# Performance work log

Measured on AMD Instinct MI355X. Metric: run time of the kernel, lower is better.

## Reference

```python
import jax, jax.numpy as jnp
import numpy as np

B, N, T, IN_DIM, OUT_DIM = 16, 500, 12, 2, 2
H, D, K, NH, NBLOCKS, T_OUT, GDEP = 64, 64, 10, 24, 2, 12, 2
H2 = 2 * H


def setup_inputs():
    key = jax.random.key(0)
    ks = iter(jax.random.split(key, 64))

    def rn(shape, s=1.0):
        return jax.random.normal(next(ks), shape, dtype=jnp.float32) * s

    def z(*shape):
        return jnp.zeros(shape, jnp.float32)

    sI = 1.0 / np.sqrt(IN_DIM)
    sH = 1.0 / np.sqrt(H)
    sH2 = 1.0 / np.sqrt(H2)
    sD = 1.0 / np.sqrt(D)
    adj = jax.random.uniform(next(ks), (N, N), dtype=jnp.float32)
    inp = {
        'x': rn((B, N, T, IN_DIM)),
        'weather': rn((B, T, 4)),
        'geo_adj': adj / adj.sum(1, keepdims=True),
        'fcx_W': rn((IN_DIM, H), sI), 'fcx_b': z(H),
        'env_cb': rn((K, D)), 'nodes_cb': rn((N, D)),
        'w_v': rn((D, K), sD), 'w_k': rn((D, D), sD), 'w_q': rn((D, D), sD),
        'core_W': rn((H, H * H), sH), 'core_b': z(H * H),
        'tcnN_Win': rn((K, H2, H2), sH2), 'tcnN_bin': z(K, H2),
        'tcnN_Wf': rn((K, NBLOCKS, 2, H2, H2), sH2), 'tcnN_bf': z(K, NBLOCKS, H2),
        'tcnN_Wg': rn((K, NBLOCKS, 2, H2, H2), sH2), 'tcnN_bg': z(K, NBLOCKS, H2),
        'tcnN_Wout': rn((K, H2, H), sH2), 'tcnN_bout': z(K, H),
        'tcnP_Win': rn((K, H2, H2), sH2), 'tcnP_bin': z(K, H2),
        'tcnP_Wf': rn((K, NBLOCKS, 2, H2, H2), sH2), 'tcnP_bf': z(K, NBLOCKS, H2),
        'tcnP_Wg': rn((K, NBLOCKS, 2, H2, H2), sH2), 'tcnP_bg': z(K, NBLOCKS, H2),
        'tcnP_Wout': rn((K, H2, H), sH2), 'tcnP_bout': z(K, H),
        'bn1_g': jnp.ones((H,), jnp.float32), 'bn1_b': z(H),
        'bnP_g': jnp.ones((H,), jnp.float32), 'bnP_b': z(H),
        'gcn1_W': rn((H, H), sH), 'gcn1_b': z(H),
        'gcn2_W': rn((H, H), sH), 'gcn2_b': z(H),
        'gcnp_W': rn((H, H), sH), 'gcnp_b': z(H),
        'nv_p1': rn((2 * NH, H)), 'nv_p2': rn((N, H)), 'nv_p3': rn((N, H)),
        'nv_pk': rn((H, H, H), sH),
        'out_W1': rn((T_OUT, H, 100), sH), 'out_b1': z(T_OUT, 100),
        'out_W2': rn((T_OUT, 100, OUT_DIM), 0.1), 'out_b2': z(T_OUT, OUT_DIM),
        't_pos': jax.random.randint(next(ks), (B, T, 2), 0, 7),
        'ind': jax.random.randint(next(ks), (B, T, 2), 0, 7),
    }
    return inp


def _tstep_emb(t, dim):
    half = dim // 2
    freqs = jnp.exp(-jnp.log(10000.0) * jnp.arange(half, dtype=jnp.float32) / half)
    a = t.astype(jnp.float32)[:, None] * freqs[None]
    return jnp.concatenate([jnp.cos(a), jnp.sin(a)], -1)


def _conv2(h, W, b, d):
    # causal kernel-2 dilated conv over time: h [B,N,T,C], W [2,C,Co] -> [B,N,T-d,Co]
    return (jnp.einsum('bntc,co->bnto', h[:, :, :-d], W[0])
            + jnp.einsum('bntc,co->bnto', h[:, :, d:], W[1]) + b)


def _tcn(xin, Win, bin_, Wf, bf, Wg, bg, Wout, bout):
    # gated dilated TCN (Graph-WaveNet style), per node over time
    h = jnp.einsum('bntc,co->bnto', xin, Win) + bin_
    for l in range(Wf.shape[0]):
        d = 2 ** l
        f = jnp.tanh(_conv2(h, Wf[l], bf[l], d))
        g = jax.nn.sigmoid(_conv2(h, Wg[l], bg[l], d))
        h = f * g + h[:, :, d:, :]
    return jnp.einsum('bntc,ch->bnth', h, Wout) + bout


def _bn(h, g, b):
    # BatchNorm1d over channels, stats over (batch, nodes); training mode
    mu = h.mean((0, 1))
    var = h.var((0, 1))
    return g * (h - mu) * jax.lax.rsqrt(var + 1e-5) + b


def _gcn(h, adj, W, b):
    # multi-hop diffusion: sum_{k=0..GDEP} A^k h, then linear
    eq = 'nm,bmh->bnh' if adj.ndim == 2 else 'bnm,bmh->bnh'
    acc, zt = h, h
    for _ in range(GDEP):
        zt = jnp.einsum(eq, adj, zt)
        acc = acc + zt
    return jnp.einsum('bnh,ho->bno', acc, W) + b


def _forward(x, weather, geo_adj, fcx_W, fcx_b, env_cb, nodes_cb, w_v, w_k, w_q,
             core_W, core_b,
             tcnN_Win, tcnN_bin, tcnN_Wf, tcnN_bf, tcnN_Wg, tcnN_bg, tcnN_Wout, tcnN_bout,
             tcnP_Win, tcnP_bin, tcnP_Wf, tcnP_bf, tcnP_Wg, tcnP_bg, tcnP_Wout, tcnP_bout,
             bn1_g, bn1_b, bnP_g, bnP_b, gcn1_W, gcn1_b, gcn2_W, gcn2_b, gcnp_W, gcnp_b,
             nv_p1, nv_p2, nv_p3, nv_pk, out_W1, out_b1, out_W2, out_b2, t_pos, ind):
    scale = 1.0 / jnp.sqrt(jnp.float32(D))
    ind_p = jnp.where(ind[:, :, 0] <= 4, ind[:, :, 1], NH - 1 + ind[:, :, 1])
    tp = jnp.where(t_pos[:, :, 0] <= 4, t_pos[:, :, 1], NH - 1 + t_pos[:, :, 1])
    t_emb = _tstep_emb(tp.reshape(-1), H).reshape(B, T, H)

    # codebook attention -> hard cluster assignment (gumbel softmax, straight-through)
    mat_v = env_cb @ w_v
    mat_k = env_cb @ w_k
    mat_q = nodes_cb @ w_q
    scores = jax.nn.softmax((mat_q @ mat_k.T) * scale, axis=1)
    logits = scores @ mat_v                                   # [N,K]
    gn = jax.random.gumbel(jax.random.key(42), logits.shape, dtype=logits.dtype)
    y_soft = jax.nn.softmax(logits + gn, axis=1)
    hard = jax.nn.one_hot(jnp.argmax(y_soft, axis=1), K, dtype=y_soft.dtype)
    mask = y_soft + jax.lax.stop_gradient(hard - y_soft)      # [N,K] one-hot fwd

    x_emb = jnp.einsum('bnti,ih->bnth', x, fcx_W) + fcx_b
    total_x = jnp.concatenate(
        [x_emb, jnp.broadcast_to(t_emb[:, None], (B, N, T, H))], -1)  # [B,N,T,2H]

    unbias = jnp.zeros((B, N, H), total_x.dtype)
    h_prev = jnp.zeros((B, N, H), total_x.dtype)
    for i in range(K):  # small fixed cluster count
        m = mask[:, i]
        xm = total_x * m[None, :, None, None]
        hn = _tcn(xm[:, :, 1:], tcnN_Win[i], tcnN_bin[i], tcnN_Wf[i], tcnN_bf[i],
                  tcnN_Wg[i], tcnN_bg[i], tcnN_Wout[i], tcnN_bout[i])[:, :, 0, :]
        hp = _tcn(xm[:, :, :-1], tcnP_Win[i], tcnP_bin[i], tcnP_Wf[i], tcnP_bf[i],
                  tcnP_Wg[i], tcnP_bg[i], tcnP_Wout[i], tcnP_bout[i])[:, :, 0, :]
        unbias = unbias + m[None, :, None] * hn
        h_prev = h_prev + m[None, :, None] * hp

    unbias = _bn(unbias, bn1_g, bn1_b)
    h_prev = _bn(h_prev, bnP_g, bnP_b)

    h1 = _gcn(h_prev, geo_adj, gcn1_W, gcn1_b)
    core = (t_emb[:, T - 1] @ core_W + core_b).reshape(B, H, H)
    causal = jax.nn.softmax(jnp.einsum('bnh,bhk,bmk->bnm', unbias, core, h_prev), axis=-1)
    h2 = _gcn(unbias, causal, gcn2_W, gcn2_b)

    te = nv_p1[ind_p[:, -(T - 1)]]                            # [B,H]
    adp = jnp.einsum('ai,ijk->ajk', te, nv_pk)
    adp = jnp.einsum('bj,ajk->abk', nv_p2, adp)
    adp = jnp.einsum('ck,abk->abc', nv_p3, adp)
    adp = jax.nn.softmax(jax.nn.relu(adp), axis=2)            # [B,N,N]
    h3 = _gcn(unbias, adp, gcnp_W, gcnp_b)

    cur_h = h1 + h2 + h3
    hmid = jax.nn.elu(jnp.einsum('bnh,thf->bntf', cur_h, out_W1) + out_b1)
    return jnp.einsum('bntf,tfo->bnto', hmid, out_W2) + out_b2  # [B,N,T_OUT,OUT_DIM]


def reference(x, weather, geo_adj, fcx_W, fcx_b, env_cb, nodes_cb, w_v, w_k, w_q,
              core_W, core_b,
              tcnN_Win, tcnN_bin, tcnN_Wf, tcnN_bf, tcnN_Wg, tcnN_bg, tcnN_Wout, tcnN_bout,
              tcnP_Win, tcnP_bin, tcnP_Wf, tcnP_bf, tcnP_Wg, tcnP_bg, tcnP_Wout, tcnP_bout,
              bn1_g, bn1_b, bnP_g, bnP_b, gcn1_W, gcn1_b, gcn2_W, gcn2_b, gcnp_W, gcnp_b,
              nv_p1, nv_p2, nv_p3, nv_pk, out_W1, out_b1, out_W2, out_b2, t_pos, ind):
    return _forward(x, weather, geo_adj, fcx_W, fcx_b, env_cb, nodes_cb, w_v, w_k, w_q,
                    core_W, core_b,
                    tcnN_Win, tcnN_bin, tcnN_Wf, tcnN_bf, tcnN_Wg, tcnN_bg, tcnN_Wout, tcnN_bout,
                    tcnP_Win, tcnP_bin, tcnP_Wf, tcnP_bf, tcnP_Wg, tcnP_bg, tcnP_Wout, tcnP_bout,
                    bn1_g, bn1_b, bnP_g, bnP_b, gcn1_W, gcn1_b, gcn2_W, gcn2_b, gcnp_W, gcnp_b,
                    nv_p1, nv_p2, nv_p3, nv_pk, out_W1, out_b1, out_W2, out_b2, t_pos, ind)
```

## Files before the change

### kernel.cpp

```cpp
#include <hip/hip_runtime.h>
#include <hip/hip_bf16.h>
#include <math.h>

#define B_ 16
#define N_ 500
#define T_ 12
#define K_ 10
#define NROWS (B_*N_)
#define TROWS 6

__device__ __forceinline__ unsigned rotl32(unsigned v, int r){ return (v<<r)|(v>>(32-r)); }

__device__ __forceinline__ void threefry2x32(unsigned k0, unsigned k1,
                                             unsigned c0, unsigned c1,
                                             unsigned &o0, unsigned &o1){
  unsigned ks2 = k0 ^ k1 ^ 0x1BD11BDAu;
  unsigned x0 = c0 + k0, x1 = c1 + k1;
#define TF_R(r) { x0 += x1; x1 = rotl32(x1,(r)); x1 ^= x0; }
  TF_R(13) TF_R(15) TF_R(26) TF_R(6)
  x0 += k1;  x1 += ks2 + 1u;
  TF_R(17) TF_R(29) TF_R(16) TF_R(24)
  x0 += ks2; x1 += k0 + 2u;
  TF_R(13) TF_R(15) TF_R(26) TF_R(6)
  x0 += k0;  x1 += k1 + 3u;
  TF_R(17) TF_R(29) TF_R(16) TF_R(24)
  x0 += k1;  x1 += ks2 + 4u;
  TF_R(13) TF_R(15) TF_R(26) TF_R(6)
  x0 += ks2; x1 += k0 + 5u;
#undef TF_R
  o0 = x0; o1 = x1;
}

__device__ __forceinline__ float gumbel_at(unsigned idx){
  unsigned b0, b1;
  threefry2x32(0u, 42u, 0u, idx, b0, b1);
  unsigned bits = b0 ^ b1;
  float u = __uint_as_float((bits >> 9) | 0x3f800000u) - 1.0f;
  u = fmaxf(u, 1.17549435e-38f);
  return -logf(-logf(u));
}

__global__ __launch_bounds__(256) void k_matq(const float* __restrict__ nodes_cb,
                                              const float* __restrict__ w_q,
                                              float* __restrict__ matq){
  int idx = blockIdx.x*256 + threadIdx.x;
  if (idx >= N_*64) return;
  int n = idx >> 6, d = idx & 63;
  float a = 0.f;
  for (int c = 0; c < 64; ++c) a += nodes_cb[n*64+c] * w_q[c*64+d];
  matq[idx] = a;
}

__global__ __launch_bounds__(256) void k_route(const float* __restrict__ env_cb,
                                               const float* __restrict__ w_v,
                                               const float* __restrict__ w_k,
                                               const float* __restrict__ matq,
                                               int* __restrict__ node_list,
                                               int* __restrict__ off){
  __shared__ float smk[K_*64];
  __shared__ float smv[K_*K_];
  __shared__ int sroute[N_];
  int tid = threadIdx.x;
  for (int idx = tid; idx < K_*64; idx += 256){
    int kk = idx >> 6, d = idx & 63;
    float a = 0.f;
    for (int c = 0; c < 64; ++c) a += env_cb[kk*64+c] * w_k[c*64+d];
    smk[idx] = a;
  }
  for (int idx = tid; idx < K_*K_; idx += 256){
    int kk = idx / K_, j = idx % K_;
    float a = 0.f;
    for (int c = 0; c < 64; ++c) a += env_cb[kk*64+c] * w_v[c*K_+j];
    smv[idx] = a;
  }
  __syncthreads();
  for (int n = tid; n < N_; n += 256){
    float s[K_];
    float mx = -1e30f;
    for (int j = 0; j < K_; ++j){
      float a = 0.f;
      for (int d = 0; d < 64; ++d) a += matq[n*64+d]*smk[j*64+d];
      s[j] = a * 0.125f;
      mx = fmaxf(mx, s[j]);
    }
    float sum = 0.f;
    for (int j = 0; j < K_; ++j){ s[j] = expf(s[j]-mx); sum += s[j]; }
    float inv = 1.f/sum;
    int best = 0; float bestv = -1e30f;
    for (int j2 = 0; j2 < K_; ++j2){
      float lg = 0.f;
      for (int j = 0; j < K_; ++j) lg += s[j]*inv*smv[j*K_+j2];
      float tot = lg + gumbel_at((unsigned)(n*K_+j2));
      if (tot > bestv){ bestv = tot; best = j2; }
    }
    sroute[n] = best;
  }
  __syncthreads();
  if (tid == 0){
    int cnt[K_]; for (int j=0;j<K_;++j) cnt[j]=0;
    for (int n=0;n<N_;++n) cnt[sroute[n]]++;
    int acc=0;
    for (int j=0;j<K_;++j){ off[j]=acc; acc+=cnt[j]; }
    off[K_]=acc;
    int pos[K_]; for (int j=0;j<K_;++j) pos[j]=off[j];
    for (int n=0;n<N_;++n) node_list[pos[sroute[n]]++] = n;
  }
}

__global__ void k_temb(const int* __restrict__ t_pos, float* __restrict__ temb){
  int tid = threadIdx.x;
  if (tid >= B_*T_) return;
  int b = tid / T_, t = tid % T_;
  int p0 = t_pos[(b*T_+t)*2+0], p1 = t_pos[(b*T_+t)*2+1];
  float tp = (float)((p0 <= 4) ? p1 : 23 + p1);
  float c0 = -logf(10000.f)/32.f;
  for (int j = 0; j < 32; ++j){
    float a = tp * expf(c0 * (float)j);
    temb[(b*T_+t)*64 + j]      = cosf(a);
    temb[(b*T_+t)*64 + 32 + j] = sinf(a);
  }
}

__global__ __launch_bounds__(256) void k_core(const float* __restrict__ temb,
                                              const float* __restrict__ core_W,
                                              const float* __restrict__ core_b,
                                              float* __restrict__ core_f){
  int idx = blockIdx.x*256 + threadIdx.x;
  if (idx >= B_*4096) return;
  int b = idx >> 12, c = idx & 4095;
  const float* te = temb + (b*T_ + 11)*64;
  float a = core_b[c];
  for (int h = 0; h < 64; ++h) a += te[h] * core_W[h*4096 + c];
  core_f[idx] = a;
}

__global__ __launch_bounds__(256) void k_tmp1(const int* __restrict__ ind,
                                              const float* __restrict__ nv_p1,
                                              const float* __restrict__ nv_pk,
                                              float* __restrict__ tmp1){
  int idx = blockIdx.x*256 + threadIdx.x;
  if (idx >= B_*4096) return;
  int b = idx >> 12, c = idx & 4095;
  int i0 = ind[(b*T_+1)*2+0], i1 = ind[(b*T_+1)*2+1];
  int row = (i0 <= 4) ? i1 : 23 + i1;
  const float* te = nv_p1 + row*64;
  float a = 0.f;
  for (int h = 0; h < 64; ++h) a += te[h] * nv_pk[h*4096 + c];
  tmp1[idx] = a;
}

__global__ __launch_bounds__(256) void k_tcn(
    const float* __restrict__ x,
    const float* __restrict__ fcx_W, const float* __restrict__ fcx_b,
    const float* __restrict__ temb,
    const int* __restrict__ node_list, const int* __restrict__ off,
    const float* __restrict__ WinN, const float* __restrict__ binN,
    const float* __restrict__ WfN,  const float* __restrict__ bfN,
    const float* __restrict__ WgN,  const float* __restrict__ bgN,
    const float* __restrict__ WoutN,const float* __restrict__ boutN,
    const float* __restrict__ WinP, const float* __restrict__ binP,
    const float* __restrict__ WfP,  const float* __restrict__ bfP,
    const float* __restrict__ WgP,  const float* __restrict__ bgP,
    const float* __restrict__ WoutP,const float* __restrict__ boutP,
    float* __restrict__ out_unb, float* __restrict__ out_hpr)
{
  int slot = blockIdx.x;
  int k = slot >> 1;
  int path = slot & 1;
  int cnt = off[k+1] - off[k];
  int rows = cnt * 16;
  int r0 = blockIdx.y * TROWS;
  if (r0 >= rows) return;

  const float* Win  = (path ? WinP  : WinN)  + k*16384;
  const float* bin  = (path ? binP  : binN)  + k*128;
  const float* Wf   = (path ? WfP   : WfN)   + k*4*16384;
  const float* bf_  = (path ? bfP   : bfN)   + k*2*128;
  const float* Wg   = (path ? WgP   : WgN)   + k*4*16384;
  const float* bg_  = (path ? bgP   : bgN)   + k*2*128;
  const float* Wout = (path ? WoutP : WoutN) + k*8192;
  const float* bout = (path ? boutP : boutN) + k*64;
  float* outb = path ? out_hpr : out_unb;
  int t0 = path ? 0 : 1;

  __shared__ __align__(16) float sIn[TROWS*512];
  __shared__ __align__(16) float sH0[TROWS*512];
  __shared__ __align__(16) float sH1[TROWS*256];
  __shared__ __align__(16) float sH2[TROWS*128];
  __shared__ int rowBN[TROWS];
  __shared__ int rowB[TROWS];

  int tid = threadIdx.x;
  if (tid < TROWS){
    int r = r0 + tid;
    if (r < rows){
      int node = node_list[off[k] + (r >> 4)];
      int b = r & 15;
      rowBN[tid] = b*N_ + node;
      rowB[tid]  = b;
    } else { rowBN[tid] = -1; rowB[tid] = 0; }
  }
  __syncthreads();

  for (int i = 0; i < TROWS; ++i){
    int rb = rowBN[i], b = rowB[i];
    for (int c2 = tid; c2 < 512; c2 += 256){
      int t = (c2 >> 7) + t0, c = c2 & 127;
      float v = 0.f;
      if (rb >= 0){
        if (c < 64){
          const float* xp = x + (rb*T_ + t)*2;
          v = xp[0]*fcx_W[c] + xp[1]*fcx_W[64+c] + fcx_b[c];
        } else {
          v = temb[(b*T_ + t)*64 + (c-64)];
        }
      }
      sIn[i*512 + c2] = v;
    }
  }
  __syncthreads();

  {
    int oc = (tid & 63)*2;
    int jg = (tid >> 6)*6;
    float a0[6], a1[6];
    #pragma unroll
    for (int j=0;j<6;++j){ a0[j]=0.f; a1[j]=0.f; }
    for (int c = 0; c < 128; c += 4){
      float2 w0 = *(const float2*)(Win + (c+0)*128 + oc);
      float2 w1 = *(const float2*)(Win + (c+1)*128 + oc);
      float2 w2 = *(const float2*)(Win + (c+2)*128 + oc);
      float2 w3 = *(const float2*)(Win + (c+3)*128 + oc);
      #pragma unroll
      for (int j=0;j<6;++j){
        float4 xv = *(const float4*)&sIn[(jg+j)*128 + c];
        a0[j] += xv.x*w0.x + xv.y*w1.x + xv.z*w2.x + xv.w*w3.x;
        a1[j] += xv.x*w0.y + xv.y*w1.y + xv.z*w2.y + xv.w*w3.y;
      }
    }
    float b0v = bin[oc], b1v = bin[oc+1];
    #pragma unroll
    for (int j=0;j<6;++j){
      sH0[(jg+j)*128 + oc]   = a0[j] + b0v;
      sH0[(jg+j)*128 + oc+1] = a1[j] + b1v;
    }
  }
  __syncthreads();

  {
    int o = tid & 127;
    int jg = (tid >> 7)*6;
    float af[6], ag[6];
    #pragma unroll
    for (int j=0;j<6;++j){ af[j]=0.f; ag[j]=0.f; }
    for (int c = 0; c < 128; c += 4){
      float f00=Wf[(c+0)*128+o], f01=Wf[(c+1)*128+o], f02=Wf[(c+2)*128+o], f03=Wf[(c+3)*128+o];
      float f10=Wf[16384+(c+0)*128+o], f11=Wf[16384+(c+1)*128+o], f12=Wf[16384+(c+2)*128+o], f13=Wf[16384+(c+3)*128+o];
      float g00=Wg[(c+0)*128+o], g01=Wg[(c+1)*128+o], g02=Wg[(c+2)*128+o], g03=Wg[(c+3)*128+o];
      float g10=Wg[16384+(c+0)*128+o], g11=Wg[16384+(c+1)*128+o], g12=Wg[16384+(c+2)*128+o], g13=Wg[16384+(c+3)*128+o];
      #pragma unroll
      for (int jj=0;jj<6;++jj){
        int j = jg + jj;
        int i = j >> 1, ti = j & 1;
        float4 xa = *(const float4*)&sH0[(i*4+ti*2  )*128 + c];
        float4 xb = *(const float4*)&sH0[(i*4+ti*2+1)*128 + c];
        af[jj] += xa.x*f00 + xa.y*f01 + xa.z*f02 + xa.w*f03
                + xb.x*f10 + xb.y*f11 + xb.z*f12 + xb.w*f13;
        ag[jj] += xa.x*g00 + xa.y*g01 + xa.z*g02 + xa.w*g03
                + xb.x*g10 + xb.y*g11 + xb.z*g12 + xb.w*g13;
      }
    }
    float bfv = bf_[o], bgv = bg_[o];
    #pragma unroll
    for (int jj=0;jj<6;++jj){
      int j = jg + jj;
      int i = j >> 1, ti = j & 1;
      float f = tanhf(af[jj] + bfv);
      float g = 1.f/(1.f + expf(-(ag[jj] + bgv)));
      sH1[j*128 + o] = f*g + sH0[(i*4 + ti*2 + 1)*128 + o];
    }
  }
  __syncthreads();

  {
    int o = tid & 127;
    int ig = (tid >> 7)*3;
    const float* Wf1 = Wf + 2*16384;
    const float* Wg1 = Wg + 2*16384;
    float af[3], ag[3];
    #pragma unroll
    for (int i=0;i<3;++i){ af[i]=0.f; ag[i]=0.f; }
    for (int c = 0; c < 128; c += 4){
      float f00=Wf1[(c+0)*128+o], f01=Wf1[(c+1)*128+o], f02=Wf1[(c+2)*128+o], f03=Wf1[(c+3)*128+o];
      float f10=Wf1[16384+(c+0)*128+o], f11=Wf1[16384+(c+1)*128+o], f12=Wf1[16384+(c+2)*128+o], f13=Wf1[16384+(c+3)*128+o];
      float g00=Wg1[(c+0)*128+o], g01=Wg1[(c+1)*128+o], g02=Wg1[(c+2)*128+o], g03=Wg1[(c+3)*128+o];
      float g10=Wg1[16384+(c+0)*128+o], g11=Wg1[16384+(c+1)*128+o], g12=Wg1[16384+(c+2)*128+o], g13=Wg1[16384+(c+3)*128+o];
      #pragma unroll
      for (int ii=0;ii<3;++ii){
        int i = ig + ii;
        float4 xa = *(const float4*)&sH1[(i*2+0)*128 + c];
        float4 xb = *(const float4*)&sH1[(i*2+1)*128 + c];
        af[ii] += xa.x*f00 + xa.y*f01 + xa.z*f02 + xa.w*f03
                + xb.x*f10 + xb.y*f11 + xb.z*f12 + xb.w*f13;
        ag[ii] += xa.x*g00 + xa.y*g01 + xa.z*g02 + xa.w*g03
                + xb.x*g10 + xb.y*g11 + xb.z*g12 + xb.w*g13;
      }
    }
    float bfv = bf_[128+o], bgv = bg_[128+o];
    #pragma unroll
    for (int ii=0;ii<3;++ii){
      int i = ig + ii;
      float f = tanhf(af[ii] + bfv);
      float g = 1.f/(1.f + expf(-(ag[ii] + bgv)));
      sH2[i*128 + o] = f*g + sH1[(i*2+1)*128 + o];
    }
  }
  __syncthreads();

  {
    int o6 = tid & 63, grp = tid >> 6;
    #pragma unroll
    for (int ii=0; ii<2; ++ii){
      int i = grp*2 + ii;
      if (i >= TROWS) continue;
      float acc = 0.f;
      for (int c = 0; c < 128; c += 4){
        float w0=Wout[(c+0)*64+o6], w1=Wout[(c+1)*64+o6],
              w2=Wout[(c+2)*64+o6], w3=Wout[(c+3)*64+o6];
        float4 xv = *(const float4*)&sH2[i*128 + c];
        acc += xv.x*w0 + xv.y*w1 + xv.z*w2 + xv.w*w3;
      }
      if (rowBN[i] >= 0) outb[rowBN[i]*64 + o6] = acc + bout[o6];
    }
  }
}

__global__ __launch_bounds__(256) void k_bnstats(const float* __restrict__ unb,
                                                 const float* __restrict__ hpr,
                                                 float* __restrict__ stats){
  int bid = blockIdx.x;
  int tensor = bid >> 6, c = bid & 63;
  const float* buf = tensor ? hpr : unb;
  float s1 = 0.f, s2 = 0.f;
  for (int r = threadIdx.x; r < NROWS; r += 256){
    float v = buf[r*64 + c];
    s1 += v; s2 += v*v;
  }
  __shared__ float r1[256], r2[256];
  r1[threadIdx.x]=s1; r2[threadIdx.x]=s2;
  __syncthreads();
  for (int s=128; s>0; s>>=1){
    if (threadIdx.x < s){ r1[threadIdx.x]+=r1[threadIdx.x+s]; r2[threadIdx.x]+=r2[threadIdx.x+s]; }
    __syncthreads();
  }
  if (threadIdx.x==0){
    float mean = r1[0]/(float)NROWS;
    float var  = r2[0]/(float)NROWS - mean*mean;
    stats[tensor*128 + c]      = mean;
    stats[tensor*128 + 64 + c] = rsqrtf(var + 1e-5f);
  }
}

__global__ __launch_bounds__(256) void k_bnapply(float* __restrict__ unb, float* __restrict__ hpr,
                                                 const float* __restrict__ stats,
                                                 const float* __restrict__ g1, const float* __restrict__ be1,
                                                 const float* __restrict__ gP, const float* __restrict__ beP){
  int idx = blockIdx.x*256 + threadIdx.x;
  if (idx >= 2*NROWS*64) return;
  int tensor = idx >= NROWS*64;
  int local = idx - tensor*NROWS*64;
  int c = local & 63;
  float* buf = tensor ? hpr : unb;
  float mean = stats[tensor*128+c], rstd = stats[tensor*128+64+c];
  float g = tensor ? gP[c] : g1[c];
  float bb = tensor ? beP[c] : be1[c];
  buf[local] = g * (buf[local]-mean) * rstd + bb;
}

template<int AMODE, int RELU, int FINAL, int ADD>
__global__ __launch_bounds__(256) void k_attn(
    const float* __restrict__ geo,
    const float* __restrict__ Qf, const float* __restrict__ Qb,
    const float* __restrict__ M,
    const float* __restrict__ Keysf, const float* __restrict__ Keysb,
    const float* __restrict__ X,
    const float* __restrict__ X0, const float* __restrict__ Z1,
    const float* __restrict__ Wg, const float* __restrict__ bg,
    float* __restrict__ cur, float* __restrict__ Y)
{
  __shared__ __align__(16) float kbuf[64][65];
  __shared__ __align__(16) float xbuf[64][64];
  __shared__ __align__(16) float vbuf[8][64];
  __shared__ __align__(16) float pbuf[8][64];

  int b = blockIdx.y, n0 = blockIdx.x*8;
  int tid = threadIdx.x;
  int nl = tid >> 5, ml = tid & 31;
  int n = n0 + nl;
  float rrK[16], rrX[16], rrA[2];

  if (AMODE != 0){
    for (int idx = tid; idx < 512; idx += 256){
      int r = idx >> 6, kk = idx & 63;
      int nn = n0 + r;
      float q = 0.f;
      if (nn < N_) q = (AMODE == 1) ? Qf[(b*N_+nn)*64+kk] : Qb[nn*64+kk];
      pbuf[r][kk] = q;
    }
    for (int idx = tid; idx < 4096; idx += 256)
      kbuf[idx>>6][idx&63] = M[b*4096 + idx];
    __syncthreads();
    float vx = 0.f, vy = 0.f;
    for (int kk = 0; kk < 64; ++kk){
      float q = pbuf[nl][kk];
      float2 m2 = *(const float2*)&kbuf[kk][ml*2];
      vx += q*m2.x; vy += q*m2.y;
    }
    __syncthreads();
    vbuf[nl][ml*2]   = vx;
    vbuf[nl][ml*2+1] = vy;
  }
  {
    if (AMODE != 0) __syncthreads();
    #pragma unroll
    for (int ii = 0; ii < 16; ++ii){
      int idx = tid + ii*256;
      int mm = idx >> 6, kk = idx & 63;
      if (AMODE != 0)
        kbuf[mm][kk] = (AMODE == 1) ? Keysf[(b*N_+mm)*64+kk] : Keysb[mm*64+kk];
      xbuf[mm][kk] = X[(b*N_+mm)*64+kk];
    }
    if (AMODE == 0){
      #pragma unroll
      for (int ii = 0; ii < 2; ++ii){
        int idx = tid + ii*256;
        int r = idx >> 6, mm = idx & 63;
        int nn = n0 + r;
        pbuf[r][mm] = (nn < N_) ? geo[nn*N_ + mm] : 0.f;
      }
    }
    __syncthreads();
  }

  float m_run = -1e30f, l_run = 0.f;
  float accx = 0.f, accy = 0.f;

  for (int ci = 0; ci < 8; ++ci){
    int m0 = ci*64;
    if (ci < 7){
      #pragma unroll
      for (int ii=0; ii<16; ++ii){
        int idx = tid + ii*256;
        int mm = idx >> 6, kk = idx & 63;
        int m = m0 + 64 + mm;
        if (AMODE != 0)
          rrK[ii] = (m < N_) ? ((AMODE == 1) ? Keysf[(b*N_+m)*64+kk] : Keysb[m*64+kk]) : 0.f;
        rrX[ii] = (m < N_) ? X[(b*N_+m)*64+kk] : 0.f;
      }
      if (AMODE == 0){
        #pragma unroll
        for (int ii=0; ii<2; ++ii){
          int idx = tid + ii*256;
          int r = idx >> 6, mm = idx & 63;
          int nn = n0 + r, m = m0 + 64 + mm;
          rrA[ii] = (nn < N_ && m < N_) ? geo[nn*N_ + m] : 0.f;
        }
      }
    }
    if (AMODE != 0){
      float s0 = 0.f, s1 = 0.f;
      for (int kk = 0; kk < 64; kk += 4){
        float4 qv = *(const float4*)&vbuf[nl][kk];
        float4 k0 = *(const float4*)&kbuf[ml   ][kk];
        float4 k1 = *(const float4*)&kbuf[ml+32][kk];
        s0 += qv.x*k0.x + qv.y*k0.y + qv.z*k0.z + qv.w*k0.w;
        s1 += qv.x*k1.x + qv.y*k1.y + qv.z*k1.z + qv.w*k1.w;
      }
      float v0 = (m0 + ml      < N_) ? (RELU ? fmaxf(s0, 0.f) : s0) : -1e30f;
      float v1 = (m0 + ml + 32 < N_) ? (RELU ? fmaxf(s1, 0.f) : s1) : -1e30f;
      float cmax = fmaxf(v0, v1);
      #pragma unroll
      for (int msk = 1; msk < 32; msk <<= 1) cmax = fmaxf(cmax, __shfl_xor(cmax, msk, 32));
      float mnew = fmaxf(m_run, cmax);
      float scale = expf(m_run - mnew);
      float p0 = expf(v0 - mnew);
      float p1 = expf(v1 - mnew);
      float lc = p0 + p1;
      #pragma unroll
      for (int msk = 1; msk < 32; msk <<= 1) lc += __shfl_xor(lc, msk, 32);
      l_run = l_run*scale + lc;
      m_run = mnew;
      accx *= scale; accy *= scale;
      pbuf[nl][ml]    = p0;
      pbuf[nl][ml+32] = p1;
    }
    __syncthreads();
    for (int mm = 0; mm < 64; mm += 4){
      float4 pv = *(const float4*)&pbuf[nl][mm];
      float2 x0 = *(const float2*)&xbuf[mm+0][ml*2];
      float2 x1 = *(const float2*)&xbuf[mm+1][ml*2];
      float2 x2 = *(const float2*)&xbuf[mm+2][ml*2];
      float2 x3 = *(const float2*)&xbuf[mm+3][ml*2];
      accx += pv.x*x0.x + pv.y*x1.x + pv.z*x2.x + pv.w*x3.x;
      accy += pv.x*x0.y + pv.y*x1.y + pv.z*x2.y + pv.w*x3.y;
    }
    __syncthreads();
    if (ci < 7){
      #pragma unroll
      for (int ii=0; ii<16; ++ii){
        int idx = tid + ii*256;
        int mm = idx >> 6, kk = idx & 63;
        if (AMODE != 0) kbuf[mm][kk] = rrK[ii];
        xbuf[mm][kk] = rrX[ii];
      }
      if (AMODE == 0){
        #pragma unroll
        for (int ii=0; ii<2; ++ii){
          int idx = tid + ii*256;
          pbuf[idx>>6][idx&63] = rrA[ii];
        }
      }
      __syncthreads();
    }
  }
  if (AMODE != 0){
    float inv = 1.f / l_run;
    accx *= inv; accy *= inv;
  }

  if (!FINAL){
    if (n < N_){
      float2 o2; o2.x = accx; o2.y = accy;
      *(float2*)&Y[(b*N_+n)*64 + ml*2] = o2;
    }
    return;
  }

  {
    int row = b*N_ + n;
    float svx = 0.f, svy = 0.f;
    if (n < N_){
      float2 x0v = *(const float2*)&X0[row*64 + ml*2];
      float2 z1v = *(const float2*)&Z1[row*64 + ml*2];
      svx = accx + x0v.x + z1v.x;
      svy = accy + x0v.y + z1v.y;
    }
    vbuf[nl][ml*2]   = svx;
    vbuf[nl][ml*2+1] = svy;
    for (int idx = tid; idx < 4096; idx += 256)
      kbuf[idx>>6][idx&63] = Wg[idx];
    __syncthreads();
    float ox = 0.f, oy = 0.f;
    for (int kk = 0; kk < 64; ++kk){
      float s = vbuf[nl][kk];
      float2 w2 = *(const float2*)&kbuf[kk][ml*2];
      ox += s*w2.x; oy += s*w2.y;
    }
    if (n < N_){
      float2 bv = *(const float2*)&bg[ml*2];
      float vx = ox + bv.x, vy = oy + bv.y;
      if (ADD){
        float2 old = *(const float2*)&cur[row*64 + ml*2];
        vx += old.x; vy += old.y;
      }
      float2 o2; o2.x = vx; o2.y = vy;
      *(float2*)&cur[row*64 + ml*2] = o2;
    }
  }
}

__global__ __launch_bounds__(128) void k_out(const float* __restrict__ cur,
                                             const float* __restrict__ W1, const float* __restrict__ bb1,
                                             const float* __restrict__ W2, const float* __restrict__ bb2,
                                             float* __restrict__ out){
  __shared__ float ch[4][64];
  __shared__ float hid[4*1200];
  int tid = threadIdx.x;
  int rbase = blockIdx.x*4;
  for (int idx = tid; idx < 256; idx += 128){
    int r = idx >> 6, h = idx & 63;
    ch[r][h] = cur[(rbase+r)*64 + h];
  }
  __syncthreads();
  for (int job = tid; job < 1200; job += 128){
    int t = job / 100, f = job - t*100;
    float a0 = bb1[t*100+f], a1 = a0, a2 = a0, a3 = a0;
    for (int h = 0; h < 64; ++h){
      float w = W1[(t*64+h)*100 + f];
      a0 += ch[0][h]*w; a1 += ch[1][h]*w; a2 += ch[2][h]*w; a3 += ch[3][h]*w;
    }
    hid[0*1200+job] = (a0 > 0.f) ? a0 : expm1f(a0);
    hid[1*1200+job] = (a1 > 0.f) ? a1 : expm1f(a1);
    hid[2*1200+job] = (a2 > 0.f) ? a2 : expm1f(a2);
    hid[3*1200+job] = (a3 > 0.f) ? a3 : expm1f(a3);
  }
  __syncthreads();
  if (tid < 96){
    int r = tid / 24, rem = tid % 24;
    int t = rem >> 1, o = rem & 1;
    float a = bb2[t*2+o];
    const float* hp = hid + r*1200 + t*100;
    for (int f = 0; f < 100; ++f) a += hp[f] * W2[(t*100+f)*2+o];
    out[(rbase+r)*24 + t*2+o] = a;
  }
}

extern "C" void kernel_launch(void* const* d_in, const int* in_sizes, int n_in,
                              void* d_out, int out_size, void* d_ws, size_t ws_size,
                              hipStream_t stream)
{
  const float* x        = (const float*)d_in[0];
  const float* geo      = (const float*)d_in[2];
  const float* fcx_W    = (const float*)d_in[3];
  const float* fcx_b    = (const float*)d_in[4];
  const float* env_cb   = (const float*)d_in[5];
  const float* nodes_cb = (const float*)d_in[6];
  const float* w_v      = (const float*)d_in[7];
  const float* w_k      = (const float*)d_in[8];
  const float* w_q      = (const float*)d_in[9];
  const float* core_W   = (const float*)d_in[10];
  const float* core_b   = (const float*)d_in[11];
  const float* tN_Win   = (const float*)d_in[12];
  const float* tN_bin   = (const float*)d_in[13];
  const float* tN_Wf    = (const float*)d_in[14];
  const float* tN_bf    = (const float*)d_in[15];
  const float* tN_Wg    = (const float*)d_in[16];
  const float* tN_bg    = (const float*)d_in[17];
  const float* tN_Wout  = (const float*)d_in[18];
  const float* tN_bout  = (const float*)d_in[19];
  const float* tP_Win   = (const float*)d_in[20];
  const float* tP_bin   = (const float*)d_in[21];
  const float* tP_Wf    = (const float*)d_in[22];
  const float* tP_bf    = (const float*)d_in[23];
  const float* tP_Wg    = (const float*)d_in[24];
  const float* tP_bg    = (const float*)d_in[25];
  const float* tP_Wout  = (const float*)d_in[26];
  const float* tP_bout  = (const float*)d_in[27];
  const float* bn1_g    = (const float*)d_in[28];
  const float* bn1_b    = (const float*)d_in[29];
  const float* bnP_g    = (const float*)d_in[30];
  const float* bnP_b    = (const float*)d_in[31];
  const float* gcn1_W   = (const float*)d_in[32];
  const float* gcn1_b   = (const float*)d_in[33];
  const float* gcn2_W   = (const float*)d_in[34];
  const float* gcn2_b   = (const float*)d_in[35];
  const float* gcnp_W   = (const float*)d_in[36];
  const float* gcnp_b   = (const float*)d_in[37];
  const float* nv_p1    = (const float*)d_in[38];
  const float* nv_p2    = (const float*)d_in[39];
  const float* nv_p3    = (const float*)d_in[40];
  const float* nv_pk    = (const float*)d_in[41];
  const float* out_W1   = (const float*)d_in[42];
  const float* out_b1   = (const float*)d_in[43];
  const float* out_W2   = (const float*)d_in[44];
  const float* out_b2   = (const float*)d_in[45];
  const int*   t_pos    = (const int*)d_in[46];
  const int*   ind      = (const int*)d_in[47];

  int* node_list = (int*)d_ws;
  int* off       = node_list + 512;
  float* F = (float*)((char*)d_ws + 4096);
  float* temb   = F + 0;
  float* core_f = F + 12288;
  float* tmp1   = F + 77824;
  float* stats  = F + 143360;
  float* matq   = F + 143616;
  float* unb    = F + 175616;
  float* hpr    = F + 687616;
  float* cur    = F + 1199616;
  float* zt1    = F + 1711616;

  k_matq <<<dim3(125), dim3(256), 0, stream>>>(nodes_cb, w_q, matq);
  k_route<<<dim3(1),   dim3(256), 0, stream>>>(env_cb, w_v, w_k, matq, node_list, off);
  k_temb <<<dim3(1),   dim3(192), 0, stream>>>(t_pos, temb);
  k_core <<<dim3(256), dim3(256), 0, stream>>>(temb, core_W, core_b, core_f);
  k_tcn  <<<dim3(20, 334), dim3(256), 0, stream>>>(x, fcx_W, fcx_b, temb, node_list, off,
      tN_Win, tN_bin, tN_Wf, tN_bf, tN_Wg, tN_bg, tN_Wout, tN_bout,
      tP_Win, tP_bin, tP_Wf, tP_bf, tP_Wg, tP_bg, tP_Wout, tP_bout,
      unb, hpr);
  k_bnstats<<<dim3(128), dim3(256), 0, stream>>>(unb, hpr, stats);
  k_bnapply<<<dim3(4000),dim3(256), 0, stream>>>(unb, hpr, stats, bn1_g, bn1_b, bnP_g, bnP_b);

  dim3 ag(64, 16);
  k_attn<0,0,0,0><<<ag, 256, 0, stream>>>(geo, nullptr,nullptr,nullptr, nullptr,nullptr,
                                 hpr, nullptr,nullptr, nullptr,nullptr, nullptr, zt1);
  k_attn<0,0,1,0><<<ag, 256, 0, stream>>>(geo, nullptr,nullptr,nullptr, nullptr,nullptr,
                                 zt1, hpr, zt1, gcn1_W, gcn1_b, cur, nullptr);
  k_attn<1,0,0,0><<<ag, 256, 0, stream>>>(nullptr, unb,nullptr, core_f, hpr,nullptr,
                                 unb, nullptr,nullptr, nullptr,nullptr, nullptr, zt1);
  k_attn<1,0,1,1><<<ag, 256, 0, stream>>>(nullptr, unb,nullptr, core_f, hpr,nullptr,
                                 zt1, unb, zt1, gcn2_W, gcn2_b, cur, nullptr);
  k_tmp1<<<dim3(256), dim3(256), 0, stream>>>(ind, nv_p1, nv_pk, tmp1);
  k_attn<2,1,0,0><<<ag, 256, 0, stream>>>(nullptr, nullptr,nv_p2, tmp1, nullptr,nv_p3,
                                 unb, nullptr,nullptr, nullptr,nullptr, nullptr, zt1);
  k_attn<2,1,1,1><<<ag, 256, 0, stream>>>(nullptr, nullptr,nv_p2, tmp1, nullptr,nv_p3,
                                 zt1, unb, zt1, gcnp_W, gcnp_b, cur, nullptr);
  k_out<<<dim3(2000), dim3(128), 0, stream>>>(cur, out_W1, out_b1, out_W2, out_b2, (float*)d_out);
}
```

Baseline: 969.6 us.

## Fuse two-hop attention GCN passes into single cooperative kernel with grid sync

Adds a cooperative kernel, k_gcn, that computes the attention probabilities for each block of 8 nodes once and keeps them in shared memory. It then runs both propagation hops, separated by a grid-wide sync, and finishes with the GCN linear projection. Each pair of k_attn launches is replaced by one cooperative launch, which avoids recomputing the score and softmax work and saves launches. The old kernels stay as a fallback if the cooperative launch fails. The design relies on all 1024 blocks being co-resident and adds the cost of a grid barrier.

```diff
diff --git a/kernel.cpp b/kernel.cpp
--- a/kernel.cpp
+++ b/kernel.cpp
@@ -1,6 +1,9 @@
 #include <hip/hip_runtime.h>
 #include <hip/hip_bf16.h>
+#include <hip/hip_cooperative_groups.h>
 #include <math.h>
+
+namespace cg = cooperative_groups;
 
 #define B_ 16
 #define N_ 500
@@ -375,6 +378,230 @@
   float g = tensor ? gP[c] : g1[c];
   float bb = tensor ? beP[c] : be1[c];
   buf[local] = g * (buf[local]-mean) * rstd + bb;
+}
+
+template<int AMODE, int RELU, int ADD>
+__global__ __launch_bounds__(256, 4) void k_gcn(
+    const float* __restrict__ geo,
+    const float* __restrict__ Qf, const float* __restrict__ Qb,
+    const float* __restrict__ M,
+    const float* __restrict__ Keysf, const float* __restrict__ Keysb,
+    const float* __restrict__ X,
+    const float* __restrict__ Wg, const float* __restrict__ bg,
+    float* __restrict__ cur, float* __restrict__ zt1)
+{
+  __shared__ float buf[64][65];
+  __shared__ float pbuf[8][516];
+  __shared__ float vbuf[8][65];
+
+  int b = blockIdx.y, n0 = blockIdx.x*8;
+  int tid = threadIdx.x;
+  int nl = tid >> 5, ml = tid & 31;
+  int n = n0 + nl;
+  float rr[16];
+
+  if (AMODE == 0){
+    for (int idx = tid; idx < 8*512; idx += 256){
+      int r = idx >> 9, m = idx & 511;
+      int nn = n0 + r;
+      pbuf[r][m] = (nn < N_ && m < N_) ? geo[nn*N_+m] : 0.f;
+    }
+    __syncthreads();
+  } else {
+    for (int idx = tid; idx < 512; idx += 256){
+      int r = idx >> 6, kk = idx & 63;
+      int nn = n0 + r;
+      float q = 0.f;
+      if (nn < N_) q = (AMODE==1) ? Qf[(b*N_+nn)*64+kk] : Qb[nn*64+kk];
+      pbuf[r][kk] = q;
+    }
+    for (int idx = tid; idx < 4096; idx += 256)
+      buf[idx>>6][idx&63] = M[b*4096+idx];
+    __syncthreads();
+    float vx=0.f, vy=0.f;
+    for (int kk = 0; kk < 64; ++kk){
+      float q = pbuf[nl][kk];
+      float2 m2 = *(const float2*)&buf[kk][ml*2];
+      vx += q*m2.x; vy += q*m2.y;
+    }
+    __syncthreads();
+    vbuf[nl][ml*2]   = vx;
+    vbuf[nl][ml*2+1] = vy;
+    #pragma unroll
+    for (int ii=0; ii<16; ++ii){
+      int idx = tid + ii*256;
+      int mm = idx>>6, kk = idx&63;
+      buf[mm][kk] = (AMODE==1) ? Keysf[(b*N_+mm)*64+kk] : Keysb[mm*64+kk];
+    }
+    __syncthreads();
+    for (int ci = 0; ci < 8; ++ci){
+      int m0 = ci*64;
+      if (ci < 7){
+        #pragma unroll
+        for (int ii=0; ii<16; ++ii){
+          int idx = tid + ii*256;
+          int mm = idx>>6, kk = idx&63;
+          int m = m0+64+mm;
+          rr[ii] = (m < N_) ? ((AMODE==1)? Keysf[(b*N_+m)*64+kk] : Keysb[m*64+kk]) : 0.f;
+        }
+      }
+      float s0=0.f, s1=0.f;
+      for (int kk = 0; kk < 64; kk += 4){
+        float4 qv = *(const float4*)&vbuf[nl][kk];
+        float4 k0 = *(const float4*)&buf[ml   ][kk];
+        float4 k1 = *(const float4*)&buf[ml+32][kk];
+        s0 += qv.x*k0.x + qv.y*k0.y + qv.z*k0.z + qv.w*k0.w;
+        s1 += qv.x*k1.x + qv.y*k1.y + qv.z*k1.z + qv.w*k1.w;
+      }
+      pbuf[nl][m0+ml]    = s0;
+      pbuf[nl][m0+ml+32] = s1;
+      __syncthreads();
+      if (ci < 7){
+        #pragma unroll
+        for (int ii=0; ii<16; ++ii){
+          int idx = tid + ii*256;
+          buf[idx>>6][idx&63] = rr[ii];
+        }
+        __syncthreads();
+      }
+    }
+    float lmax = -1e30f;
+    for (int m = ml; m < 512; m += 32){
+      float v = pbuf[nl][m];
+      if (m < N_){ if (RELU) v = fmaxf(v, 0.f); } else v = -1e30f;
+      lmax = fmaxf(lmax, v);
+    }
+    #pragma unroll
+    for (int msk=1; msk<32; msk<<=1) lmax = fmaxf(lmax, __shfl_xor(lmax, msk, 32));
+    float lsum = 0.f;
+    for (int m = ml; m < 512; m += 32){
+      float v = pbuf[nl][m];
+      float p = 0.f;
+      if (m < N_){ if (RELU) v = fmaxf(v, 0.f); p = expf(v - lmax); }
+      pbuf[nl][m] = p;
+      lsum += p;
+    }
+    #pragma unroll
+    for (int msk=1; msk<32; msk<<=1) lsum += __shfl_xor(lsum, msk, 32);
+    float inv = 1.f/lsum;
+    for (int m = ml; m < 512; m += 32) pbuf[nl][m] *= inv;
+    __syncthreads();
+  }
+
+  float accx = 0.f, accy = 0.f;
+  #pragma unroll
+  for (int ii=0; ii<16; ++ii){
+    int idx = tid + ii*256;
+    int mm = idx>>6, kk = idx&63;
+    buf[mm][kk] = X[(b*N_+mm)*64+kk];
+  }
+  __syncthreads();
+  for (int ci = 0; ci < 8; ++ci){
+    int m0 = ci*64;
+    if (ci < 7){
+      #pragma unroll
+      for (int ii=0; ii<16; ++ii){
+        int idx = tid + ii*256;
+        int mm = idx>>6, kk = idx&63;
+        int m = m0+64+mm;
+        rr[ii] = (m < N_) ? X[(b*N_+m)*64+kk] : 0.f;
+      }
+    }
+    for (int mm = 0; mm < 64; mm += 4){
+      float4 pv = *(const float4*)&pbuf[nl][m0+mm];
+      float2 x0 = *(const float2*)&buf[mm+0][ml*2];
+      float2 x1 = *(const float2*)&buf[mm+1][ml*2];
+      float2 x2 = *(const float2*)&buf[mm+2][ml*2];
+      float2 x3 = *(const float2*)&buf[mm+3][ml*2];
+      accx += pv.x*x0.x + pv.y*x1.x + pv.z*x2.x + pv.w*x3.x;
+      accy += pv.x*x0.y + pv.y*x1.y + pv.z*x2.y + pv.w*x3.y;
+    }
+    __syncthreads();
+    if (ci < 7){
+      #pragma unroll
+      for (int ii=0; ii<16; ++ii){
+        int idx = tid + ii*256;
+        buf[idx>>6][idx&63] = rr[ii];
+      }
+      __syncthreads();
+    }
+  }
+  if (n < N_){
+    float2 o2; o2.x = accx; o2.y = accy;
+    *(float2*)&zt1[(b*N_+n)*64 + ml*2] = o2;
+  }
+  __threadfence();
+  cg::this_grid().sync();
+
+  float a2x = 0.f, a2y = 0.f;
+  #pragma unroll
+  for (int ii=0; ii<16; ++ii){
+    int idx = tid + ii*256;
+    int mm = idx>>6, kk = idx&63;
+    buf[mm][kk] = zt1[(b*N_+mm)*64+kk];
+  }
+  __syncthreads();
+  for (int ci = 0; ci < 8; ++ci){
+    int m0 = ci*64;
+    if (ci < 7){
+      #pragma unroll
+      for (int ii=0; ii<16; ++ii){
+        int idx = tid + ii*256;
+        int mm = idx>>6, kk = idx&63;
+        int m = m0+64+mm;
+        rr[ii] = (m < N_) ? zt1[(b*N_+m)*64+kk] : 0.f;
+      }
+    }
+    for (int mm = 0; mm < 64; mm += 4){
+      float4 pv = *(const float4*)&pbuf[nl][m0+mm];
+      float2 x0 = *(const float2*)&buf[mm+0][ml*2];
+      float2 x1 = *(const float2*)&buf[mm+1][ml*2];
+      float2 x2 = *(const float2*)&buf[mm+2][ml*2];
+      float2 x3 = *(const float2*)&buf[mm+3][ml*2];
+      a2x += pv.x*x0.x + pv.y*x1.x + pv.z*x2.x + pv.w*x3.x;
+      a2y += pv.x*x0.y + pv.y*x1.y + pv.z*x2.y + pv.w*x3.y;
+    }
+    __syncthreads();
+    if (ci < 7){
+      #pragma unroll
+      for (int ii=0; ii<16; ++ii){
+        int idx = tid + ii*256;
+        buf[idx>>6][idx&63] = rr[ii];
+      }
+      __syncthreads();
+    }
+  }
+
+  {
+    int row = b*N_ + n;
+    float svx = 0.f, svy = 0.f;
+    if (n < N_){
+      float2 xv = *(const float2*)&X[row*64 + ml*2];
+      svx = a2x + accx + xv.x;
+      svy = a2y + accy + xv.y;
+    }
+    vbuf[nl][ml*2]   = svx;
+    vbuf[nl][ml*2+1] = svy;
+    for (int idx = tid; idx < 4096; idx += 256)
+      buf[idx>>6][idx&63] = Wg[idx];
+    __syncthreads();
+    float ox = 0.f, oy = 0.f;
+    for (int kk = 0; kk < 64; ++kk){
+      float s = vbuf[nl][kk];
+      float2 w2 = *(const float2*)&buf[kk][ml*2];
+      ox += s*w2.x; oy += s*w2.y;
+    }
+    if (n < N_){
+      float2 bv = *(const float2*)&bg[ml*2];
+      float vx2 = ox + bv.x, vy2 = oy + bv.y;
+      if (ADD){
+        float2 old = *(const float2*)&cur[row*64 + ml*2];
+        vx2 += old.x; vy2 += old.y;
+      }
+      float2 o2; o2.x = vx2; o2.y = vy2;
+      *(float2*)&cur[row*64 + ml*2] = o2;
+    }
+  }
 }
 
 template<int AMODE, int RELU, int FINAL, int ADD>
@@ -680,20 +907,50 @@
       unb, hpr);
   k_bnstats<<<dim3(128), dim3(256), 0, stream>>>(unb, hpr, stats);
   k_bnapply<<<dim3(4000),dim3(256), 0, stream>>>(unb, hpr, stats, bn1_g, bn1_b, bnP_g, bnP_b);
-
+  k_tmp1<<<dim3(256), dim3(256), 0, stream>>>(ind, nv_p1, nv_pk, tmp1);
+
+  dim3 cgrid(64, 16), cblock(256);
+  const float* nil = nullptr;
   dim3 ag(64, 16);
-  k_attn<0,0,0,0><<<ag, 256, 0, stream>>>(geo, nullptr,nullptr,nullptr, nullptr,nullptr,
-                                 hpr, nullptr,nullptr, nullptr,nullptr, nullptr, zt1);
-  k_attn<0,0,1,0><<<ag, 256, 0, stream>>>(geo, nullptr,nullptr,nullptr, nullptr,nullptr,
-                                 zt1, hpr, zt1, gcn1_W, gcn1_b, cur, nullptr);
-  k_attn<1,0,0,0><<<ag, 256, 0, stream>>>(nullptr, unb,nullptr, core_f, hpr,nullptr,
-                                 unb, nullptr,nullptr, nullptr,nullptr, nullptr, zt1);
-  k_attn<1,0,1,1><<<ag, 256, 0, stream>>>(nullptr, unb,nullptr, core_f, hpr,nullptr,
-                                 zt1, unb, zt1, gcn2_W, gcn2_b, cur, nullptr);
-  k_tmp1<<<dim3(256), dim3(256), 0, stream>>>(ind, nv_p1, nv_pk, tmp1);
-  k_attn<2,1,0,0><<<ag, 256, 0, stream>>>(nullptr, nullptr,nv_p2, tmp1, nullptr,nv_p3,
-                                 unb, nullptr,nullptr, nullptr,nullptr, nullptr, zt1);
-  k_attn<2,1,1,1><<<ag, 256, 0, stream>>>(nullptr, nullptr,nv_p2, tmp1, nullptr,nv_p3,
-                                 zt1, unb, zt1, gcnp_W, gcnp_b, cur, nullptr);
+
+  {
+    const float* aG=geo, *aQf=nil, *aQb=nil, *aM=nil, *aKf=nil, *aKb=nil, *aX=hpr,
+               * aW=gcn1_W, *aB=gcn1_b;
+    float *aC=cur, *aZ=zt1;
+    void* args[] = {&aG,&aQf,&aQb,&aM,&aKf,&aKb,&aX,&aW,&aB,&aC,&aZ};
+    if (hipLaunchCooperativeKernel((const void*)k_gcn<0,0,0>, cgrid, cblock, args, 0, stream)
+        != hipSuccess){
+      k_attn<0,0,0,0><<<ag, 256, 0, stream>>>(geo, nil,nil,nil, nil,nil,
+                                     hpr, nil,nil, nil,nil, nullptr, zt1);
+      k_attn<0,0,1,0><<<ag, 256, 0, stream>>>(geo, nil,nil,nil, nil,nil,
+                                     zt1, hpr, zt1, gcn1_W, gcn1_b, cur, nullptr);
+    }
+  }
+  {
+    const float* aG=nil, *aQf=unb, *aQb=nil, *aM=core_f, *aKf=hpr, *aKb=nil, *aX=unb,
+               * aW=gcn2_W, *aB=gcn2_b;
+    float *aC=cur, *aZ=zt1;
+    void* args[] = {&aG,&aQf,&aQb,&aM,&aKf,&aKb,&aX,&aW,&aB,&aC,&aZ};
+    if (hipLaunchCooperativeKernel((const void*)k_gcn<1,0,1>, cgrid, cblock, args, 0, stream)
+        != hipSuccess){
+      k_attn<1,0,0,0><<<ag, 256, 0, stream>>>(nil, unb,nil, core_f, hpr,nil,
+                                     unb, nil,nil, nil,nil, nullptr, zt1);
+      k_attn<1,0,1,1><<<ag, 256, 0, stream>>>(nil, unb,nil, core_f, hpr,nil,
+                                     zt1, unb, zt1, gcn2_W, gcn2_b, cur, nullptr);
+    }
+  }
+  {
+    const float* aG=nil, *aQf=nil, *aQb=nv_p2, *aM=tmp1, *aKf=nil, *aKb=nv_p3, *aX=unb,
+               * aW=gcnp_W, *aB=gcnp_b;
+    float *aC=cur, *aZ=zt1;
+    void* args[] = {&aG,&aQf,&aQb,&aM,&aKf,&aKb,&aX,&aW,&aB,&aC,&aZ};
+    if (hipLaunchCooperativeKernel((const void*)k_gcn<2,1,1>, cgrid, cblock, args, 0, stream)
+        != hipSuccess){
+      k_attn<2,1,0,0><<<ag, 256, 0, stream>>>(nil, nil,nv_p2, tmp1, nil,nv_p3,
+                                     unb, nil,nil, nil,nil, nullptr, zt1);
+      k_attn<2,1,1,1><<<ag, 256, 0, stream>>>(nil, nil,nv_p2, tmp1, nil,nv_p3,
+                                     zt1, unb, zt1, gcnp_W, gcnp_b, cur, nullptr);
+    }
+  }
   k_out<<<dim3(2000), dim3(128), 0, stream>>>(cur, out_W1, out_b1, out_W2, out_b2, (float*)d_out);
 }
```

Result: slower. 1.613 ms (+66.3%).
